# Kernel tuning notes

Measured on AMD Instinct MI355X. Metric: run time of the kernel, lower is better.

## Reference

```python
import jax, jax.numpy as jnp
import numpy as np

N, E = 50000, 800000
IN_DIM, H0, H1, OUT_DIM = 64, 64, 64, 8
NUM_RELS, NUM_BASES = 16, 8


def setup_inputs() -> dict:
    key = jax.random.key(0)
    ks = jax.random.split(key, 20)
    features = jax.random.normal(ks[0], (N, IN_DIM), dtype=jnp.float32)
    etypes = jax.random.randint(ks[1], (E,), 0, NUM_RELS)
    src = jax.random.randint(ks[2], (E,), 0, N)
    dst = jax.random.randint(ks[3], (E,), 0, N)
    # degree normalization 1/in_degree(dst), as DGL stores in g.edata['norm']
    deg = jax.ops.segment_sum(jnp.ones((E,), jnp.float32), dst, num_segments=N)
    norm = (1.0 / jnp.maximum(deg, 1.0))[dst][:, None]  # [E,1]

    def glorot(k, shape):
        fan_in, fan_out = shape[-2], shape[-1]
        lim = jnp.sqrt(6.0 / (fan_in + fan_out)).astype(jnp.float32)
        return jax.random.uniform(k, shape, jnp.float32, -lim, lim)

    dims = [(IN_DIM, H0), (H0, H1), (H1, OUT_DIM)]
    inp = {"features": features, "norm": norm}
    for i, (di, do) in enumerate(dims):
        inp[f"basis{i}"] = glorot(ks[4 + 4 * i], (NUM_BASES, di, do))
        inp[f"comp{i}"] = glorot(ks[5 + 4 * i], (NUM_RELS, NUM_BASES))
        inp[f"loop{i}"] = glorot(ks[6 + 4 * i], (di, do))
        inp[f"bias{i}"] = jnp.zeros((do,), jnp.float32)
    inp["etypes"] = etypes
    inp["src"] = src
    inp["dst"] = dst
    return inp


def rel_graph_conv(h, basis, comp, loop_w, bias, etypes, src, dst, norm, act):
    # basis-decomposed relation weights: [R, din, dout]
    W = jnp.einsum('rb,bio->rio', comp, basis)
    # transform every node under every relation: [N, R, dout]
    h_trans = jnp.einsum('ni,rio->nro', h, W)
    # per-edge gather of (src node, edge relation), degree-normalized
    msg = h_trans[src, etypes] * norm  # [E, dout]
    agg = jax.ops.segment_sum(msg, dst, num_segments=h.shape[0])  # [N, dout]
    out = agg + h @ loop_w + bias  # self-loop + bias (DGL defaults)
    return act(out)


def reference(features, norm, basis0, comp0, loop0, bias0, basis1, comp1, loop1,
              bias1, basis2, comp2, loop2, bias2, etypes, src, dst):
    lrelu = lambda x: jax.nn.leaky_relu(x, negative_slope=0.01)
    h = rel_graph_conv(features, basis0, comp0, loop0, bias0, etypes, src, dst, norm, lrelu)
    h = rel_graph_conv(h, basis1, comp1, loop1, bias1, etypes, src, dst, norm, lrelu)
    h = rel_graph_conv(h, basis2, comp2, loop2, bias2, etypes, src, dst, norm, jax.nn.relu)
    return h
```

## Files before the change

kernel.cpp:

```cpp
#include <hip/hip_runtime.h>

#define NN 50000
#define NE 800000
#define CAP 64
#define KC 72
#define CSTR 16

typedef __bf16 bf16x8 __attribute__((ext_vector_type(8)));
typedef float f32x4 __attribute__((ext_vector_type(4)));
typedef unsigned short ushort;
typedef unsigned int uint;

__device__ inline ushort f2bf(float x) {
  uint u = __builtin_bit_cast(uint, x);
  u += 0x7FFF + ((u >> 16) & 1);
  return (ushort)(u >> 16);
}
__device__ inline float bf2f(ushort u) {
  return __builtin_bit_cast(float, (uint)u << 16);
}


__device__ inline void wprep_body(const float* __restrict__ basis,
                                  const float* __restrict__ loopw,
                                  ushort* __restrict__ W2, int DOUT, int NCOLS,
                                  int idx) {
  int total = KC * NCOLS * 8;
  if (idx >= total) return;
  int j = idx & 7;
  int n = (idx >> 3) % NCOLS;
  int kc = idx / (8 * NCOLS);
  int k = kc * 8 + j;
  float v = 0.f;
  if (n < DOUT) v = (k < 512) ? basis[k * DOUT + n] : loopw[(k - 512) * DOUT + n];
  W2[((size_t)kc * NCOLS + n) * 8 + j] = f2bf(v);
}

__global__ __launch_bounds__(256) void build_kernel(
    const int* __restrict__ dstv, const int* __restrict__ srcv,
    const int* __restrict__ etv, int* __restrict__ cursor, int* __restrict__ pk,
    const float* __restrict__ f, ushort* __restrict__ fb,
    const float* __restrict__ b0, const float* __restrict__ l0, ushort* __restrict__ W0,
    const float* __restrict__ b1, const float* __restrict__ l1, ushort* __restrict__ W1,
    const float* __restrict__ b2, const float* __restrict__ l2, ushort* __restrict__ W2,
    const float* __restrict__ c0, const float* __restrict__ c1,
    const float* __restrict__ c2, float* __restrict__ cp) {
  int blk = blockIdx.x;
  int tid = threadIdx.x;
  if (blk < 3125) {
    int i = blk * 256 + tid;
    int d = dstv[i];
    int p = atomicAdd(&cursor[(size_t)d * CSTR], 1);
    if (p < CAP) pk[d * CAP + p] = (etv[i] << 16) | srcv[i];
  } else if (blk < 6250) {
    int i = (blk - 3125) * 256 + tid;
    float4 v = ((const float4*)f)[i];
    ushort4 u;
    u.x = f2bf(v.x); u.y = f2bf(v.y); u.z = f2bf(v.z); u.w = f2bf(v.w);
    ((ushort4*)fb)[i] = u;
  } else if (blk < 6394) {
    wprep_body(b0, l0, W0, 64, 64, (blk - 6250) * 256 + tid);
  } else if (blk < 6538) {
    wprep_body(b1, l1, W1, 64, 64, (blk - 6394) * 256 + tid);
  } else if (blk < 6574) {
    wprep_body(b2, l2, W2, 8, 16, (blk - 6538) * 256 + tid);
  } else {
    int idx = (blk - 6574) * 256 + tid;
    if (idx < 408) {
      int l = idx / 136, k = idx % 136;
      const float* src = (l == 0) ? c0 : ((l == 1) ? c1 : c2);
      cp[idx] = (k < 128) ? src[k] : 0.f;
    }
  }
}


template <int DOUT, int NCOLS, bool OBF>
__global__ __launch_bounds__(1024, 8) void layer_kernel(
    const ushort* __restrict__ hb,
    const float* __restrict__ cpad,
    const int* __restrict__ degv,
    const int* __restrict__ pk,
    const ushort* __restrict__ W2,
    const float* __restrict__ bias,
    void* __restrict__ outp,
    float slope)
{
  __shared__ ushort X[KC][16][8];
  int tid = threadIdx.x;
  int wave = tid >> 6;
  int lane = tid & 63;
  int dbase = blockIdx.x * 16;
  int d = __builtin_amdgcn_readfirstlane(dbase + wave);

  int deg = degv[(size_t)d * CSTR];
  int dw = deg > CAP ? CAP : deg;
  const int4* p4 = (const int4*)(pk + (size_t)d * CAP);

  float acc[8] = {0.f, 0.f, 0.f, 0.f, 0.f, 0.f, 0.f, 0.f};
  for (int base = 0; base < dw; base += 16) {
    int qg = base >> 2;
    int4 e0 = p4[qg + 0];
    int4 e1 = p4[qg + 1];
    int4 e2 = p4[qg + 2];
    int4 e3 = p4[qg + 3];
    int pe[16] = {e0.x, e0.y, e0.z, e0.w, e1.x, e1.y, e1.z, e1.w,
                  e2.x, e2.y, e2.z, e2.w, e3.x, e3.y, e3.z, e3.w};
#pragma unroll
    for (int i = 0; i < 16; ++i) {
      int p = __builtin_amdgcn_readfirstlane(pe[i]);
      p = (base + i < dw) ? p : (16 << 16);
      float hv = bf2f(hb[(size_t)(p & 0xFFFF) * 64 + lane]);
      const float* c = cpad + (p >> 16) * 8;
#pragma unroll
      for (int b = 0; b < 8; ++b) acc[b] = fmaf(c[b], hv, acc[b]);
    }
  }

  float inv = 1.0f / (float)(deg > 1 ? deg : 1);
  int jj = lane & 7;
  int csub = lane >> 3;
#pragma unroll
  for (int b = 0; b < 8; ++b) X[b * 8 + csub][wave][jj] = f2bf(acc[b] * inv);
  X[64 + csub][wave][jj] = hb[(size_t)d * 64 + lane];
  __syncthreads();

  if (wave < (DOUT == 64 ? 4 : 1)) {
    int q = lane >> 4;
    int r = lane & 15;
    f32x4 acc2 = {0.f, 0.f, 0.f, 0.f};
#pragma unroll
    for (int ks = 0; ks < 18; ++ks) {
      int kc = ks * 4 + q;
      bf16x8 bfrag = *(const bf16x8*)&X[kc][r][0];
      bf16x8 afrag = *(const bf16x8*)(W2 + ((size_t)kc * NCOLS + wave * 16 + r) * 8);
      acc2 = __builtin_amdgcn_mfma_f32_16x16x32_bf16(afrag, bfrag, acc2, 0, 0, 0);
    }
    int m = dbase + r;
    int nb = wave * 16 + q * 4;
    if (nb < DOUT) {
      float4 bv = *(const float4*)(bias + nb);
      float v0 = acc2[0] + bv.x;
      float v1 = acc2[1] + bv.y;
      float v2 = acc2[2] + bv.z;
      float v3 = acc2[3] + bv.w;
      v0 = v0 > 0.f ? v0 : slope * v0;
      v1 = v1 > 0.f ? v1 : slope * v1;
      v2 = v2 > 0.f ? v2 : slope * v2;
      v3 = v3 > 0.f ? v3 : slope * v3;
      if (OBF) {
        ushort4 u;
        u.x = f2bf(v0); u.y = f2bf(v1); u.z = f2bf(v2); u.w = f2bf(v3);
        *(ushort4*)((ushort*)outp + (size_t)m * DOUT + nb) = u;
      } else {
        *(float4*)((float*)outp + (size_t)m * DOUT + nb) = float4{v0, v1, v2, v3};
      }
    }
  }
}


extern "C" void kernel_launch(void* const* d_in, const int* in_sizes, int n_in,
                              void* d_out, int out_size, void* d_ws, size_t ws_size,
                              hipStream_t stream) {
  const float* features = (const float*)d_in[0];
  const float* basis0   = (const float*)d_in[2];
  const float* comp0    = (const float*)d_in[3];
  const float* loop0    = (const float*)d_in[4];
  const float* bias0    = (const float*)d_in[5];
  const float* basis1   = (const float*)d_in[6];
  const float* comp1    = (const float*)d_in[7];
  const float* loop1    = (const float*)d_in[8];
  const float* bias1    = (const float*)d_in[9];
  const float* basis2   = (const float*)d_in[10];
  const float* comp2    = (const float*)d_in[11];
  const float* loop2    = (const float*)d_in[12];
  const float* bias2    = (const float*)d_in[13];
  const int* etypes     = (const int*)d_in[14];
  const int* srcv       = (const int*)d_in[15];
  const int* dstv       = (const int*)d_in[16];

  char* ws = (char*)d_ws;
  size_t off = 0;
  auto alloc = [&](size_t bytes) {
    void* p = ws + off;
    off += (bytes + 255) & ~(size_t)255;
    return p;
  };
  int* cnt      = (int*)alloc((size_t)NN * CSTR * sizeof(int));
  int* pk       = (int*)alloc((size_t)NN * CAP * sizeof(int));
  ushort* W2_0  = (ushort*)alloc((size_t)KC * 64 * 8 * sizeof(ushort));
  ushort* W2_1  = (ushort*)alloc((size_t)KC * 64 * 8 * sizeof(ushort));
  ushort* W2_2  = (ushort*)alloc((size_t)KC * 16 * 8 * sizeof(ushort));
  float* cpad   = (float*)alloc(3 * 136 * sizeof(float));
  ushort* fbf   = (ushort*)alloc((size_t)NN * 64 * sizeof(ushort));
  ushort* hA    = (ushort*)alloc((size_t)NN * 64 * sizeof(ushort));
  ushort* hB    = (ushort*)alloc((size_t)NN * 64 * sizeof(ushort));

  hipMemsetAsync(cnt, 0, (size_t)NN * CSTR * sizeof(int), stream);
  build_kernel<<<6576, 256, 0, stream>>>(dstv, srcv, etypes, cnt, pk,
                                         features, fbf,
                                         basis0, loop0, W2_0,
                                         basis1, loop1, W2_1,
                                         basis2, loop2, W2_2,
                                         comp0, comp1, comp2, cpad);

  layer_kernel<64, 64, true><<<3125, 1024, 0, stream>>>(
      fbf, cpad + 0 * 136, cnt, pk, W2_0, bias0, hA, 0.01f);
  layer_kernel<64, 64, true><<<3125, 1024, 0, stream>>>(
      hA, cpad + 1 * 136, cnt, pk, W2_1, bias1, hB, 0.01f);
  layer_kernel<8, 16, false><<<3125, 1024, 0, stream>>>(
      hB, cpad + 2 * 136, cnt, pk, W2_2, bias2, d_out, 0.0f);
}
```

Before: 192.2 us.

## Batch gathers, use packed FMA accumulation, and XOR-swizzle shared tile

The edge loop now processes 8 edges per iteration, issuing all eight feature gathers before doing the accumulation, so several loads are in flight at once. The accumulation uses packed two-wide float FMAs over the per-relation coefficients. The shared-memory X tile is XOR-swizzled on the row index to reduce LDS bank conflicts on the MFMA B-fragment reads. The smaller edge batch and the extra live registers may affect occupancy or add loop overhead.

Result: faster. 175.9 us (-8.5%).

```diff
diff --git a/kernel.cpp b/kernel.cpp
--- a/kernel.cpp
+++ b/kernel.cpp
@@ -8,6 +8,7 @@
 
 typedef __bf16 bf16x8 __attribute__((ext_vector_type(8)));
 typedef float f32x4 __attribute__((ext_vector_type(4)));
+typedef float f32x2 __attribute__((ext_vector_type(2)));
 typedef unsigned short ushort;
 typedef unsigned int uint;
 
@@ -97,23 +98,27 @@
   int dw = deg > CAP ? CAP : deg;
   const int4* p4 = (const int4*)(pk + (size_t)d * CAP);
 
-  float acc[8] = {0.f, 0.f, 0.f, 0.f, 0.f, 0.f, 0.f, 0.f};
-  for (int base = 0; base < dw; base += 16) {
-    int qg = base >> 2;
-    int4 e0 = p4[qg + 0];
-    int4 e1 = p4[qg + 1];
-    int4 e2 = p4[qg + 2];
-    int4 e3 = p4[qg + 3];
-    int pe[16] = {e0.x, e0.y, e0.z, e0.w, e1.x, e1.y, e1.z, e1.w,
-                  e2.x, e2.y, e2.z, e2.w, e3.x, e3.y, e3.z, e3.w};
-#pragma unroll
-    for (int i = 0; i < 16; ++i) {
-      int p = __builtin_amdgcn_readfirstlane(pe[i]);
-      p = (base + i < dw) ? p : (16 << 16);
-      float hv = bf2f(hb[(size_t)(p & 0xFFFF) * 64 + lane]);
-      const float* c = cpad + (p >> 16) * 8;
-#pragma unroll
-      for (int b = 0; b < 8; ++b) acc[b] = fmaf(c[b], hv, acc[b]);
+  f32x2 acc2[4] = {{0.f, 0.f}, {0.f, 0.f}, {0.f, 0.f}, {0.f, 0.f}};
+  for (int base = 0; base < dw; base += 8) {
+    int qg = base >> 3;
+    int4 e0 = p4[qg * 2];
+    int4 e1 = p4[qg * 2 + 1];
+    int pe[8] = {e0.x, e0.y, e0.z, e0.w, e1.x, e1.y, e1.z, e1.w};
+    float hv[8];
+    int ps[8];
+#pragma unroll
+    for (int i = 0; i < 8; ++i) {
+      int pr = __builtin_amdgcn_readfirstlane(pe[i]);
+      ps[i] = (base + i < dw) ? pr : (16 << 16);
+      hv[i] = bf2f(hb[(size_t)(ps[i] & 0xFFFF) * 64 + lane]);
+    }
+#pragma unroll
+    for (int i = 0; i < 8; ++i) {
+      const f32x2* c2 = (const f32x2*)(cpad + (ps[i] >> 16) * 8);
+      f32x2 h2 = {hv[i], hv[i]};
+#pragma unroll
+      for (int j = 0; j < 4; ++j)
+        acc2[j] = __builtin_elementwise_fma(c2[j], h2, acc2[j]);
     }
   }
 
@@ -121,29 +126,32 @@
   int jj = lane & 7;
   int csub = lane >> 3;
 #pragma unroll
-  for (int b = 0; b < 8; ++b) X[b * 8 + csub][wave][jj] = f2bf(acc[b] * inv);
-  X[64 + csub][wave][jj] = hb[(size_t)d * 64 + lane];
+  for (int b = 0; b < 8; ++b) {
+    float v = ((b & 1) ? acc2[b >> 1].y : acc2[b >> 1].x) * inv;
+    X[b * 8 + csub][wave ^ csub][jj] = f2bf(v);
+  }
+  X[64 + csub][wave ^ csub][jj] = hb[(size_t)d * 64 + lane];
   __syncthreads();
 
   if (wave < (DOUT == 64 ? 4 : 1)) {
     int q = lane >> 4;
     int r = lane & 15;
-    f32x4 acc2 = {0.f, 0.f, 0.f, 0.f};
+    f32x4 accd = {0.f, 0.f, 0.f, 0.f};
 #pragma unroll
     for (int ks = 0; ks < 18; ++ks) {
       int kc = ks * 4 + q;
-      bf16x8 bfrag = *(const bf16x8*)&X[kc][r][0];
+      bf16x8 bfrag = *(const bf16x8*)&X[kc][r ^ (kc & 7)][0];
       bf16x8 afrag = *(const bf16x8*)(W2 + ((size_t)kc * NCOLS + wave * 16 + r) * 8);
-      acc2 = __builtin_amdgcn_mfma_f32_16x16x32_bf16(afrag, bfrag, acc2, 0, 0, 0);
+      accd = __builtin_amdgcn_mfma_f32_16x16x32_bf16(afrag, bfrag, accd, 0, 0, 0);
     }
     int m = dbase + r;
     int nb = wave * 16 + q * 4;
     if (nb < DOUT) {
       float4 bv = *(const float4*)(bias + nb);
-      float v0 = acc2[0] + bv.x;
-      float v1 = acc2[1] + bv.y;
-      float v2 = acc2[2] + bv.z;
-      float v3 = acc2[3] + bv.w;
+      float v0 = accd[0] + bv.x;
+      float v1 = accd[1] + bv.y;
+      float v2 = accd[2] + bv.z;
+      float v3 = accd[3] + bv.w;
       v0 = v0 > 0.f ? v0 : slope * v0;
       v1 = v1 > 0.f ? v1 : slope * v1;
       v2 = v2 > 0.f ? v2 : slope * v2;
```
